# Kernel optimization log

Hardware: AMD Instinct MI355X
Metric: run time of the kernel (lower is better)

Reference implementation:

```python
import jax, jax.numpy as jnp
from jax import lax
import numpy as np

B, T = 32, 64
E = 64        # embed_dim
U = 32        # num_measurements
D0, D1 = 300, 100
S = 9         # speaker_num
CELL = 64     # output_cell_dim
C = 6         # n_classes
EPS = 1e-12


def setup_inputs() -> dict:
    key = jax.random.key(0)
    ks = jax.random.split(key, 16)
    sc = 1.0 / np.sqrt(E)
    n = lambda i, shape, s=1.0: (jax.random.normal(ks[i], shape, jnp.float32) * s)
    return {
        "x0": n(0, (B, T, D0)),
        "x1": n(1, (B, T, D1)),
        "smask": jax.random.uniform(ks[2], (B, T, S), jnp.float32),
        "umask": jnp.ones((B, T), jnp.float32),
        "W_ih0": n(3, (4 * E, D0), sc), "W_hh0": n(4, (4 * E, E), sc),
        "b_ih0": n(5, (4 * E,), sc), "b_hh0": n(6, (4 * E,), sc),
        "W_ih1": n(7, (4 * E, D1), sc), "W_hh1": n(8, (4 * E, E), sc),
        "b_ih1": n(9, (4 * E,), sc), "b_hh1": n(10, (4 * E,), sc),
        "phase_table": jax.random.uniform(ks[11], (S, E), jnp.float32, -np.pi, np.pi),
        "meas_kernel": jax.random.uniform(ks[12], (U, E, 2), jnp.float32),
        "W1": n(13, (CELL, 2 * U), 0.1), "b1": jnp.zeros((CELL,), jnp.float32),
        "W2": n(14, (C, CELL), 0.1), "b2": jnp.zeros((C,), jnp.float32),
    }


def _lstm_tanh(x, um, Wih, Whh, bih, bhh):
    # torch.nn.LSTMCell (gate order i,f,g,o) + extra tanh applied to h each step;
    # the tanh-ed h is carried as the recurrent state (dropout = identity in eval).
    b, t, _ = x.shape
    e = Whh.shape[1]

    def step(carry, inp):
        h, c = carry
        xt, ut = inp
        g = (xt * ut[:, None]) @ Wih.T + bih + h @ Whh.T + bhh
        i, f, gg, o = jnp.split(g, 4, axis=-1)
        c = jax.nn.sigmoid(f) * c + jax.nn.sigmoid(i) * jnp.tanh(gg)
        h = jnp.tanh(jax.nn.sigmoid(o) * jnp.tanh(c))
        return (h, c), h

    h0 = jnp.zeros((b, e), x.dtype)
    _, hs = lax.scan(step, (h0, h0), (jnp.swapaxes(x, 0, 1), um.T))
    return jnp.swapaxes(hs, 0, 1)  # (B,T,E)


def _measure(amp, phase, kernel):
    # pure state v = cos(phase)*amp + i sin(phase)*amp; rho = |v><v|
    r = jnp.cos(phase) * amp
    im = jnp.sin(phase) * amp
    rho_r = jnp.einsum('bti,btj->btij', r, r) + jnp.einsum('bti,btj->btij', im, im)
    rho_i = jnp.einsum('bti,btj->btij', im, r) - jnp.einsum('bti,btj->btij', r, im)
    u = kernel.shape[0]
    norm = jnp.clip(jnp.linalg.norm(kernel.reshape(u, -1), axis=-1), EPS)
    kn = kernel / norm[:, None, None]
    kr, ki = kn[..., 0], kn[..., 1]
    Pr = jnp.einsum('ui,uj->uij', kr, kr) + jnp.einsum('ui,uj->uij', ki, ki)
    Pi = jnp.einsum('ui,uj->uij', ki, kr) - jnp.einsum('ui,uj->uij', kr, ki)
    return jnp.einsum('btij,uij->btu', rho_r, Pr) - jnp.einsum('btij,uij->btu', rho_i, Pi)


def reference(x0, x1, smask, umask, W_ih0, W_hh0, b_ih0, b_hh0,
              W_ih1, W_hh1, b_ih1, b_hh1, phase_table, meas_kernel,
              W1, b1, W2, b2):
    h0 = _lstm_tanh(x0, umask, W_ih0, W_hh0, b_ih0, b_hh0)
    h1 = _lstm_tanh(x1, umask, W_ih1, W_hh1, b_ih1, b_hh1)
    norm = lambda h: h / jnp.clip(jnp.linalg.norm(h, axis=-1, keepdims=True), EPS)
    phase = phase_table[jnp.argmax(smask, axis=-1)]  # (B,T,E); table shared by both modalities
    m = jnp.concatenate([_measure(norm(h0), phase, meas_kernel),
                         _measure(norm(h1), phase, meas_kernel)], axis=-1)
    hid = jax.nn.relu(m @ W1.T + b1)
    pred = jnp.tanh(hid @ W2.T + b2)
    return jax.nn.log_softmax(pred, axis=2)
```

## Files before the change

kernel.cpp:

```cpp
#include <hip/hip_runtime.h>

typedef unsigned short ushort_t;
typedef unsigned int uint_t;
typedef float f32x2 __attribute__((ext_vector_type(2)));

__device__ __forceinline__ float bf2f(ushort_t v) {
  union { uint_t u; float f; } x; x.u = ((uint_t)v) << 16; return x.f;
}
__device__ __forceinline__ float lo16(uint_t u) {
  union { uint_t u; float f; } x; x.u = u << 16; return x.f;
}
__device__ __forceinline__ float hi16(uint_t u) {
  union { uint_t u; float f; } x; x.u = u & 0xffff0000u; return x.f;
}
__device__ __forceinline__ ushort_t f2bf(float f) {
  union { float f; uint_t u; } x; x.f = f;
  uint_t u = x.u;
  uint_t r = (u + 0x7fffu + ((u >> 16) & 1u)) >> 16;
  return (ushort_t)r;
}
__device__ __forceinline__ bool is_bf16(const void* um) {
  return *(const uint_t*)um == 0x3F803F80u;
}
__device__ __forceinline__ float ld_dual(const void* p, int i, bool isb) {
  return isb ? bf2f(((const ushort_t*)p)[i]) : ((const float*)p)[i];
}
__device__ __forceinline__ float fsig(float x) { return 1.f / (1.f + __expf(-x)); }
__device__ __forceinline__ float ftanh(float x) { return 2.f / (1.f + __expf(-2.f * x)) - 1.f; }

#if defined(__has_builtin)
#if __has_builtin(__builtin_elementwise_fma)
#define FMA2(a, b, c) __builtin_elementwise_fma((a), (b), (c))
#endif
#endif
#ifndef FMA2
__device__ __forceinline__ f32x2 fma2_fb(f32x2 a, f32x2 b, f32x2 c) {
  c.x = fmaf(a.x, b.x, c.x); c.y = fmaf(a.y, b.y, c.y); return c;
}
#define FMA2(a, b, c) fma2_fb((a), (b), (c))
#endif

__device__ __forceinline__ float dpp_add_xor1(float v) {
  const int r = __builtin_amdgcn_update_dpp(0, __float_as_int(v), 0xB1, 0xF, 0xF, true);
  return v + __int_as_float(r);
}
__device__ __forceinline__ float dpp_add_xor2(float v) {
  const int r = __builtin_amdgcn_update_dpp(0, __float_as_int(v), 0x4E, 0xF, 0xF, true);
  return v + __int_as_float(r);
}

template <int D, bool ISB>
__device__ __forceinline__ void proj_body(
    const void* __restrict__ x, const void* __restrict__ um,
    const void* __restrict__ Wih, const void* __restrict__ bih,
    const void* __restrict__ bhh, float* __restrict__ xw)
{
  const int g = threadIdx.x;
  const int r0 = blockIdx.x * 4;
  float acc[4] = {0.f, 0.f, 0.f, 0.f};
  const float* xf = (const float*)x;
  const ushort_t* xh = (const ushort_t*)x;
#pragma unroll 2
  for (int k = 0; k < D; k += 4) {
    float w0, w1, w2, w3;
    if (ISB) {
      const uint2 wu = *(const uint2*)((const ushort_t*)Wih + g * D + k);
      w0 = lo16(wu.x); w1 = hi16(wu.x); w2 = lo16(wu.y); w3 = hi16(wu.y);
    } else {
      const float4 wv = *(const float4*)((const float*)Wih + g * D + k);
      w0 = wv.x; w1 = wv.y; w2 = wv.z; w3 = wv.w;
    }
#pragma unroll
    for (int r = 0; r < 4; ++r) {
      float xa, xb, xc, xd;
      if (ISB) {
        const uint2 xu = *(const uint2*)(xh + (r0 + r) * D + k);
        xa = lo16(xu.x); xb = hi16(xu.x); xc = lo16(xu.y); xd = hi16(xu.y);
      } else {
        const float4 xv = *(const float4*)(xf + (r0 + r) * D + k);
        xa = xv.x; xb = xv.y; xc = xv.z; xd = xv.w;
      }
      acc[r] = fmaf(xa, w0, acc[r]);
      acc[r] = fmaf(xb, w1, acc[r]);
      acc[r] = fmaf(xc, w2, acc[r]);
      acc[r] = fmaf(xd, w3, acc[r]);
    }
  }
  const float bias = ld_dual(bih, g, ISB) + ld_dual(bhh, g, ISB);
  const int pos = ((g & 63) << 2) | (g >> 6);
#pragma unroll
  for (int r = 0; r < 4; ++r) {
    const float u = ld_dual(um, r0 + r, ISB);
    xw[(r0 + r) * 256 + pos] = fmaf(acc[r], u, bias);
  }
}

__global__ __launch_bounds__(256) void proj_both(
    const void* __restrict__ x0, const void* __restrict__ x1,
    const void* __restrict__ um,
    const void* __restrict__ Wih0, const void* __restrict__ bih0,
    const void* __restrict__ bhh0,
    const void* __restrict__ Wih1, const void* __restrict__ bih1,
    const void* __restrict__ bhh1,
    float* __restrict__ xw0, float* __restrict__ xw1)
{
  const bool isb = is_bf16(um);
  if (blockIdx.y == 0) {
    if (isb) proj_body<300, true>(x0, um, Wih0, bih0, bhh0, xw0);
    else     proj_body<300, false>(x0, um, Wih0, bih0, bhh0, xw0);
  } else {
    if (isb) proj_body<100, true>(x1, um, Wih1, bih1, bhh1, xw1);
    else     proj_body<100, false>(x1, um, Wih1, bih1, bhh1, xw1);
  }
}

__global__ __launch_bounds__(256, 1) void lstm_k(
    const float* __restrict__ xw0, const float* __restrict__ xw1,
    const void* __restrict__ Whh0, const void* __restrict__ Whh1,
    const void* __restrict__ um,
    float* __restrict__ h0r, float* __restrict__ h1r)
{
  __shared__ __align__(16) float xws[64 * 256];
  __shared__ __align__(16) float hist[65 * 64];

  const int bid = blockIdx.x;
  const int l = bid >> 5;
  const int b = bid & 31;
  const float* xw = (l ? xw1 : xw0) + b * 64 * 256;
  const void* Whh = (l ? Whh1 : Whh0);
  float* hr = (l ? h1r : h0r) + b * 64 * 64;
  const int tid = threadIdx.x;
  const int e = tid >> 2;
  const int q = tid & 3;
  const int k0 = q << 4;
  const bool isb = is_bf16(um);

  for (int i = tid; i < 4096; i += 256)
    *(float4*)(xws + i * 4) = *(const float4*)(xw + i * 4);
  if (tid < 64) hist[tid] = 0.f;

  f32x2 w2[4][8];
  if (isb) {
#pragma unroll
    for (int t = 0; t < 4; ++t) {
      const ushort_t* wr = (const ushort_t*)Whh + (t * 64 + e) * 64 + k0;
#pragma unroll
      for (int j = 0; j < 16; j += 8) {
        const uint4 v = *(const uint4*)(wr + j);
        w2[t][(j >> 1) + 0] = f32x2{lo16(v.x), hi16(v.x)};
        w2[t][(j >> 1) + 1] = f32x2{lo16(v.y), hi16(v.y)};
        w2[t][(j >> 1) + 2] = f32x2{lo16(v.z), hi16(v.z)};
        w2[t][(j >> 1) + 3] = f32x2{lo16(v.w), hi16(v.w)};
      }
    }
  } else {
#pragma unroll
    for (int t = 0; t < 4; ++t) {
      const float* wr = (const float*)Whh + (t * 64 + e) * 64 + k0;
#pragma unroll
      for (int j = 0; j < 16; j += 4) {
        const float4 v = *(const float4*)(wr + j);
        w2[t][(j >> 1) + 0] = f32x2{v.x, v.y};
        w2[t][(j >> 1) + 1] = f32x2{v.z, v.w};
      }
    }
  }
  __syncthreads();

  float c = 0.f;
  for (int s = 0; s < 64; ++s) {
    const float gin = xws[s * 256 + tid];
    const float* hp = hist + s * 64 + k0;
    f32x2 P0 = {0.f, 0.f}, P1 = {0.f, 0.f}, P2 = {0.f, 0.f}, P3 = {0.f, 0.f};
#pragma unroll
    for (int j = 0; j < 16; j += 4) {
      const float4 hv = *(const float4*)(hp + j);
      const f32x2 hA = {hv.x, hv.y}, hB = {hv.z, hv.w};
      const int jp = j >> 1;
      P0 = FMA2(w2[0][jp], hA, P0); P0 = FMA2(w2[0][jp + 1], hB, P0);
      P1 = FMA2(w2[1][jp], hA, P1); P1 = FMA2(w2[1][jp + 1], hB, P1);
      P2 = FMA2(w2[2][jp], hA, P2); P2 = FMA2(w2[2][jp + 1], hB, P2);
      P3 = FMA2(w2[3][jp], hA, P3); P3 = FMA2(w2[3][jp + 1], hB, P3);
    }
    float p0 = P0.x + P0.y;
    float p1 = P1.x + P1.y;
    float p2 = P2.x + P2.y;
    float p3 = P3.x + P3.y;
    if (q == 0) p0 += gin;
    else if (q == 1) p1 += gin;
    else if (q == 2) p2 += gin;
    else p3 += gin;
    p0 = dpp_add_xor1(p0); p0 = dpp_add_xor2(p0);
    p1 = dpp_add_xor1(p1); p1 = dpp_add_xor2(p1);
    p2 = dpp_add_xor1(p2); p2 = dpp_add_xor2(p2);
    p3 = dpp_add_xor1(p3); p3 = dpp_add_xor2(p3);
    const float yi = fsig(p0);
    const float yf = fsig(p1);
    const float yg = ftanh(p2);
    const float yo = fsig(p3);
    c = fmaf(yf, c, yi * yg);
    const float h = ftanh(yo * ftanh(c));
    if (q == 0) hist[(s + 1) * 64 + e] = h;
    __syncthreads();
  }
  for (int i = tid; i < 1024; i += 256)
    *(float4*)(hr + i * 4) = *(const float4*)(hist + 64 + i * 4);
}

__global__ __launch_bounds__(256) void head_k(
    const float* __restrict__ h0r, const float* __restrict__ h1r,
    const void* __restrict__ smask, const void* __restrict__ um,
    const void* __restrict__ ptab, const void* __restrict__ mker,
    const void* __restrict__ W1, const void* __restrict__ b1,
    const void* __restrict__ W2, const void* __restrict__ b2,
    void* __restrict__ out)
{
  __shared__ float2 knT[64][32];
  __shared__ float w1T[64][65];
  __shared__ float w2T[64][9];
  __shared__ float b1s[64];
  __shared__ float b2s[8];
  __shared__ float rim[4][4][64];
  __shared__ float msh[4][64];
  __shared__ float hidsh[4][64];
  __shared__ float psh[4][8];

  const int tid = threadIdx.x;
  const bool isb = is_bf16(um);
  {
    const int u = tid >> 3, sub = tid & 7;
    float vr[8], vi[8];
    float ssq = 0.f;
#pragma unroll
    for (int qq = 0; qq < 8; ++qq) {
      const int e = sub * 8 + qq;
      if (isb) {
        const uint_t kk = ((const uint_t*)mker)[u * 64 + e];
        vr[qq] = lo16(kk); vi[qq] = hi16(kk);
      } else {
        const float2 kk = ((const float2*)mker)[u * 64 + e];
        vr[qq] = kk.x; vi[qq] = kk.y;
      }
      ssq = fmaf(vr[qq], vr[qq], ssq);
      ssq = fmaf(vi[qq], vi[qq], ssq);
    }
    ssq += __shfl_xor(ssq, 1);
    ssq += __shfl_xor(ssq, 2);
    ssq += __shfl_xor(ssq, 4);
    const float rn = 1.f / fmaxf(sqrtf(ssq), 1e-12f);
#pragma unroll
    for (int qq = 0; qq < 8; ++qq) {
      const int e = sub * 8 + qq;
      knT[e][u] = make_float2(vr[qq] * rn, vi[qq] * rn);
    }
  }
  for (int i = tid; i < 4096; i += 256) {
    const int j = i >> 6, ll = i & 63;
    w1T[ll][j] = ld_dual(W1, i, isb);
  }
  if (tid < 64) b1s[tid] = ld_dual(b1, tid, isb);
  for (int i = tid; i < 384; i += 256) {
    const int cc = i >> 6, j = i & 63;
    w2T[j][cc] = ld_dual(W2, i, isb);
  }
  if (tid < 6) b2s[tid] = ld_dual(b2, tid, isb);
  __syncthreads();

  const int wv = tid >> 6, lane = tid & 63;
  const int item = blockIdx.x * 4 + wv;
  const float h0raw = h0r[item * 64 + lane];
  const float h1raw = h1r[item * 64 + lane];
  float ss0 = h0raw * h0raw, ss1 = h1raw * h1raw;
#pragma unroll
  for (int m = 1; m < 64; m <<= 1) {
    ss0 += __shfl_xor(ss0, m);
    ss1 += __shfl_xor(ss1, m);
  }
  const float h0 = h0raw / fmaxf(sqrtf(ss0), 1e-12f);
  const float h1 = h1raw / fmaxf(sqrtf(ss1), 1e-12f);

  int idx = 0;
  if (lane == 0) {
    float best = -1e30f;
#pragma unroll
    for (int si = 0; si < 9; ++si) {
      const float v = ld_dual(smask, item * 9 + si, isb);
      if (v > best) { best = v; idx = si; }
    }
  }
  idx = __shfl(idx, 0, 64);
  const float ph = ld_dual(ptab, idx * 64 + lane, isb);
  float sr, cr;
  __sincosf(ph, &sr, &cr);
  rim[wv][0][lane] = cr * h0;
  rim[wv][1][lane] = sr * h0;
  rim[wv][2][lane] = cr * h1;
  rim[wv][3][lane] = sr * h1;
  __syncthreads();
  {
    const int u = lane & 31;
    const float* ra = rim[wv][(lane >= 32) ? 2 : 0];
    const float* ia = rim[wv][(lane >= 32) ? 3 : 1];
    float ar = 0.f, ai = 0.f;
#pragma unroll 8
    for (int e = 0; e < 64; ++e) {
      const float2 k = knT[e][u];
      const float rr = ra[e], ii = ia[e];
      ar = fmaf(rr, k.x, ar);
      ar = fmaf(-ii, k.y, ar);
      ai = fmaf(rr, k.y, ai);
      ai = fmaf(ii, k.x, ai);
    }
    msh[wv][lane] = fmaf(ar, ar, ai * ai);
  }
  __syncthreads();
  {
    float acc = b1s[lane];
#pragma unroll 8
    for (int L = 0; L < 64; ++L)
      acc = fmaf(msh[wv][L], w1T[L][lane], acc);
    hidsh[wv][lane] = fmaxf(acc, 0.f);
  }
  __syncthreads();
  if (lane < 6) {
    float a2 = b2s[lane];
#pragma unroll 8
    for (int j = 0; j < 64; ++j)
      a2 = fmaf(hidsh[wv][j], w2T[j][lane], a2);
    psh[wv][lane] = ftanh(a2);
  }
  __syncthreads();
  if (lane < 6) {
    const float p = psh[wv][lane];
    float mx = psh[wv][0];
#pragma unroll
    for (int cc = 1; cc < 6; ++cc) mx = fmaxf(mx, psh[wv][cc]);
    float sum = 0.f;
#pragma unroll
    for (int cc = 0; cc < 6; ++cc) sum += __expf(psh[wv][cc] - mx);
    const float res = p - mx - __logf(sum);
    if (isb) ((ushort_t*)out)[item * 6 + lane] = f2bf(res);
    else     ((float*)out)[item * 6 + lane] = res;
  }
}

extern "C" void kernel_launch(void* const* d_in, const int* in_sizes, int n_in,
                              void* d_out, int out_size, void* d_ws, size_t ws_size,
                              hipStream_t stream)
{
  (void)in_sizes; (void)n_in; (void)out_size; (void)ws_size;
  const void* x0    = d_in[0];
  const void* x1    = d_in[1];
  const void* smask = d_in[2];
  const void* um    = d_in[3];
  const void* Wih0  = d_in[4];
  const void* Whh0  = d_in[5];
  const void* bih0  = d_in[6];
  const void* bhh0  = d_in[7];
  const void* Wih1  = d_in[8];
  const void* Whh1  = d_in[9];
  const void* bih1  = d_in[10];
  const void* bhh1  = d_in[11];
  const void* ptab  = d_in[12];
  const void* mker  = d_in[13];
  const void* W1    = d_in[14];
  const void* b1    = d_in[15];
  const void* W2    = d_in[16];
  const void* b2    = d_in[17];

  float* xw0 = (float*)d_ws;
  float* xw1 = xw0 + 2048 * 256;
  float* h0r = xw1 + 2048 * 256;
  float* h1r = h0r + 2048 * 64;

  hipLaunchKernelGGL(proj_both, dim3(512, 2), dim3(256), 0, stream,
                     x0, x1, um, Wih0, bih0, bhh0, Wih1, bih1, bhh1,
                     xw0, xw1);
  hipLaunchKernelGGL(lstm_k, dim3(64), dim3(256), 0, stream,
                     xw0, xw1, Whh0, Whh1, um, h0r, h1r);
  hipLaunchKernelGGL(head_k, dim3(512), dim3(256), 0, stream,
                     h0r, h1r, smask, um, ptab, mker, W1, b1, W2, b2,
                     d_out);
}
```

Before: 181.2 us.

## Tile input projection GEMM through shared memory with 32x32 output tiles

Rewrites the input-projection kernel from a per-thread gate-row dot product over 4 rows into a shared-memory tiled GEMM. Each block stages 32 rows of x and 32 rows of W_ih in LDS in K-chunks of 100, and each thread computes a 2x2 register tile. The goal is to cut redundant global loads of the weight matrix and to improve load coalescing. The cost is extra LDS traffic and two barriers per K chunk. The projection is likely a small part of total time next to the serial LSTM kernel.

```diff
diff --git a/kernel.cpp b/kernel.cpp
--- a/kernel.cpp
+++ b/kernel.cpp
@@ -49,50 +49,71 @@
   return v + __int_as_float(r);
 }
 
+#define PROJ_LDW 108
+
 template <int D, bool ISB>
 __device__ __forceinline__ void proj_body(
     const void* __restrict__ x, const void* __restrict__ um,
     const void* __restrict__ Wih, const void* __restrict__ bih,
-    const void* __restrict__ bhh, float* __restrict__ xw)
+    const void* __restrict__ bhh, float* __restrict__ xw,
+    int rtile, int gtile, float* __restrict__ xs, float* __restrict__ ws)
 {
-  const int g = threadIdx.x;
-  const int r0 = blockIdx.x * 4;
-  float acc[4] = {0.f, 0.f, 0.f, 0.f};
-  const float* xf = (const float*)x;
-  const ushort_t* xh = (const ushort_t*)x;
-#pragma unroll 2
-  for (int k = 0; k < D; k += 4) {
-    float w0, w1, w2, w3;
-    if (ISB) {
-      const uint2 wu = *(const uint2*)((const ushort_t*)Wih + g * D + k);
-      w0 = lo16(wu.x); w1 = hi16(wu.x); w2 = lo16(wu.y); w3 = hi16(wu.y);
-    } else {
-      const float4 wv = *(const float4*)((const float*)Wih + g * D + k);
-      w0 = wv.x; w1 = wv.y; w2 = wv.z; w3 = wv.w;
-    }
-#pragma unroll
-    for (int r = 0; r < 4; ++r) {
-      float xa, xb, xc, xd;
+  const int tid = threadIdx.x;
+  const int r0 = rtile * 32;
+  const int g0 = gtile * 32;
+  const int rt = tid >> 4;
+  const int gt = tid & 15;
+  float a00 = 0.f, a01 = 0.f, a10 = 0.f, a11 = 0.f;
+
+  for (int kt = 0; kt < D; kt += 100) {
+    for (int i = tid; i < 800; i += 256) {
+      const int r = i / 25;
+      const int k4 = (i - r * 25) * 4;
       if (ISB) {
-        const uint2 xu = *(const uint2*)(xh + (r0 + r) * D + k);
-        xa = lo16(xu.x); xb = hi16(xu.x); xc = lo16(xu.y); xd = hi16(xu.y);
+        const uint2 xv = *(const uint2*)((const ushort_t*)x + (r0 + r) * D + kt + k4);
+        *(float4*)(xs + r * PROJ_LDW + k4) =
+            make_float4(lo16(xv.x), hi16(xv.x), lo16(xv.y), hi16(xv.y));
+        const uint2 wv = *(const uint2*)((const ushort_t*)Wih + (g0 + r) * D + kt + k4);
+        *(float4*)(ws + r * PROJ_LDW + k4) =
+            make_float4(lo16(wv.x), hi16(wv.x), lo16(wv.y), hi16(wv.y));
       } else {
-        const float4 xv = *(const float4*)(xf + (r0 + r) * D + k);
-        xa = xv.x; xb = xv.y; xc = xv.z; xd = xv.w;
+        *(float4*)(xs + r * PROJ_LDW + k4) =
+            *(const float4*)((const float*)x + (r0 + r) * D + kt + k4);
+        *(float4*)(ws + r * PROJ_LDW + k4) =
+            *(const float4*)((const float*)Wih + (g0 + r) * D + kt + k4);
       }
-      acc[r] = fmaf(xa, w0, acc[r]);
-      acc[r] = fmaf(xb, w1, acc[r]);
-      acc[r] = fmaf(xc, w2, acc[r]);
-      acc[r] = fmaf(xd, w3, acc[r]);
-    }
-  }
-  const float bias = ld_dual(bih, g, ISB) + ld_dual(bhh, g, ISB);
-  const int pos = ((g & 63) << 2) | (g >> 6);
-#pragma unroll
-  for (int r = 0; r < 4; ++r) {
-    const float u = ld_dual(um, r0 + r, ISB);
-    xw[(r0 + r) * 256 + pos] = fmaf(acc[r], u, bias);
-  }
+    }
+    __syncthreads();
+#pragma unroll 5
+    for (int k = 0; k < 100; k += 4) {
+      const float4 xa = *(const float4*)(xs + rt * PROJ_LDW + k);
+      const float4 xb = *(const float4*)(xs + (rt + 16) * PROJ_LDW + k);
+      const float4 wa = *(const float4*)(ws + gt * PROJ_LDW + k);
+      const float4 wb = *(const float4*)(ws + (gt + 16) * PROJ_LDW + k);
+      a00 = fmaf(xa.x, wa.x, a00); a00 = fmaf(xa.y, wa.y, a00);
+      a00 = fmaf(xa.z, wa.z, a00); a00 = fmaf(xa.w, wa.w, a00);
+      a01 = fmaf(xa.x, wb.x, a01); a01 = fmaf(xa.y, wb.y, a01);
+      a01 = fmaf(xa.z, wb.z, a01); a01 = fmaf(xa.w, wb.w, a01);
+      a10 = fmaf(xb.x, wa.x, a10); a10 = fmaf(xb.y, wa.y, a10);
+      a10 = fmaf(xb.z, wa.z, a10); a10 = fmaf(xb.w, wa.w, a10);
+      a11 = fmaf(xb.x, wb.x, a11); a11 = fmaf(xb.y, wb.y, a11);
+      a11 = fmaf(xb.z, wb.z, a11); a11 = fmaf(xb.w, wb.w, a11);
+    }
+    __syncthreads();
+  }
+
+  const int ra = r0 + rt, rb = ra + 16;
+  const int ga = g0 + gt, gb = ga + 16;
+  const float ba = ld_dual(bih, ga, ISB) + ld_dual(bhh, ga, ISB);
+  const float bb = ld_dual(bih, gb, ISB) + ld_dual(bhh, gb, ISB);
+  const float ua = ld_dual(um, ra, ISB);
+  const float ub = ld_dual(um, rb, ISB);
+  const int pa = ((ga & 63) << 2) | (ga >> 6);
+  const int pb = ((gb & 63) << 2) | (gb >> 6);
+  xw[ra * 256 + pa] = fmaf(a00, ua, ba);
+  xw[ra * 256 + pb] = fmaf(a01, ua, bb);
+  xw[rb * 256 + pa] = fmaf(a10, ub, ba);
+  xw[rb * 256 + pb] = fmaf(a11, ub, bb);
 }
 
 __global__ __launch_bounds__(256) void proj_both(
@@ -104,13 +125,20 @@
     const void* __restrict__ bhh1,
     float* __restrict__ xw0, float* __restrict__ xw1)
 {
+  __shared__ __align__(16) float xs[32 * PROJ_LDW];
+  __shared__ __align__(16) float ws[32 * PROJ_LDW];
   const bool isb = is_bf16(um);
-  if (blockIdx.y == 0) {
-    if (isb) proj_body<300, true>(x0, um, Wih0, bih0, bhh0, xw0);
-    else     proj_body<300, false>(x0, um, Wih0, bih0, bhh0, xw0);
+  const int bid = blockIdx.x;
+  const int l = bid >> 9;
+  const int t = bid & 511;
+  const int rtile = t >> 3;
+  const int gtile = t & 7;
+  if (l == 0) {
+    if (isb) proj_body<300, true>(x0, um, Wih0, bih0, bhh0, xw0, rtile, gtile, xs, ws);
+    else     proj_body<300, false>(x0, um, Wih0, bih0, bhh0, xw0, rtile, gtile, xs, ws);
   } else {
-    if (isb) proj_body<100, true>(x1, um, Wih1, bih1, bhh1, xw1);
-    else     proj_body<100, false>(x1, um, Wih1, bih1, bhh1, xw1);
+    if (isb) proj_body<100, true>(x1, um, Wih1, bih1, bhh1, xw1, rtile, gtile, xs, ws);
+    else     proj_body<100, false>(x1, um, Wih1, bih1, bhh1, xw1, rtile, gtile, xs, ws);
   }
 }
 
@@ -373,7 +401,7 @@
   float* h0r = xw1 + 2048 * 256;
   float* h1r = h0r + 2048 * 64;
 
-  hipLaunchKernelGGL(proj_both, dim3(512, 2), dim3(256), 0, stream,
+  hipLaunchKernelGGL(proj_both, dim3(1024), dim3(256), 0, stream,
                      x0, x1, um, Wih0, bih0, bhh0, Wih1, bih1, bhh1,
                      xw0, xw1);
   hipLaunchKernelGGL(lstm_k, dim3(64), dim3(256), 0, stream,
```

Result: faster. 156.1 us (-13.8%).
